# Kernel optimization log

Hardware: AMD Instinct MI355X
Metric: run time of the kernel (lower is better)

Reference implementation:

```python
import jax, jax.numpy as jnp
import numpy as np

TAU = 1.0


def setup_inputs() -> dict:
    key = jax.random.key(0)
    k1, k2 = jax.random.split(key)
    z = jax.random.normal(k1, (131072, 64), dtype=jnp.float32)
    cluster_centers = jax.random.normal(k2, (512, 64), dtype=jnp.float32)
    return {"z": z, "cluster_centers": cluster_centers}


def reference(z, cluster_centers):
    # ||z - c||^2 = ||z||^2 + ||c||^2 - 2 z.c  (avoids the [B,K,D] broadcast tensor)
    z_sq = jnp.sum(z * z, axis=1, keepdims=True)              # [B, 1]
    c_sq = jnp.sum(cluster_centers * cluster_centers, axis=1)  # [K]
    cross = jnp.einsum('bd,kd->bk', z, cluster_centers)        # [B, K]
    dist_sq = z_sq + c_sq[None, :] - 2.0 * cross               # [B, K]
    q = jax.nn.softmax(-dist_sq / TAU, axis=1)                 # [B, K]
    loss = jnp.mean(jnp.sum(q * dist_sq, axis=1))
    return (q, loss)
```

## Files before the change

kernel.cpp:

```cpp
#include <hip/hip_runtime.h>

typedef short bf16x8 __attribute__((ext_vector_type(8)));
typedef float f32x4 __attribute__((ext_vector_type(4)));

#define K_CLUSTERS 512
#define DIM 64
#define ROWS_PER_BLOCK 64

__device__ __forceinline__ unsigned short f32_to_bf16_rne(float f) {
    unsigned int u = __float_as_uint(f);
    u += 0x7fffu + ((u >> 16) & 1u);
    return (unsigned short)(u >> 16);
}
__device__ __forceinline__ float bf16_bits_to_f32(unsigned short h) {
    return __uint_as_float(((unsigned int)h) << 16);
}

__global__ void prep_centers(const float* __restrict__ c,
                             short* __restrict__ c_hi, short* __restrict__ c_lo,
                             float* __restrict__ c_sq, float* __restrict__ loss_out) {
    if (blockIdx.x == 0 && threadIdx.x == 0) loss_out[0] = 0.0f;
    int idx = blockIdx.x * 256 + threadIdx.x;
    float v = c[idx];
    unsigned short h = f32_to_bf16_rne(v);
    float hf = bf16_bits_to_f32(h);
    unsigned short l = f32_to_bf16_rne(v - hf);
    c_hi[idx] = (short)h;
    c_lo[idx] = (short)l;
    float s = v * v;
    #pragma unroll
    for (int off = 1; off < 64; off <<= 1) s += __shfl_xor(s, off, 64);
    if ((threadIdx.x & 63) == 0) c_sq[idx >> 6] = s;
}

#define BARRIER() do {                                      \
    asm volatile("s_waitcnt lgkmcnt(0)" ::: "memory");      \
    __builtin_amdgcn_s_barrier();                           \
} while (0)

__global__ __launch_bounds__(512, 4)
void cluster_kernel(const float* __restrict__ z,
                    const short* __restrict__ c_hi,
                    const short* __restrict__ c_lo,
                    const float* __restrict__ c_sq,
                    float* __restrict__ q_out,
                    float* __restrict__ loss_out,
                    float inv_b) {
    __shared__ __align__(16) short a_hi_s[16][72];
    __shared__ __align__(16) short a_lo_s[16][72];
    __shared__ __align__(16) float2 red_s[8][16];
    __shared__ float wloss_s[8];

    const int tid  = threadIdx.x;
    const int lane = tid & 63;
    const int wave = tid >> 6;
    const int m    = lane & 15;
    const int qd   = lane >> 4;
    const long rb  = (long)blockIdx.x * ROWS_PER_BLOCK;

    bf16x8 bh[4][2], bl[4][2];
    float csq[4];
    #pragma unroll
    for (int t = 0; t < 4; ++t) {
        const int col = wave * 64 + t * 16 + m;
        const long boff = (long)col * DIM + qd * 8;
        #pragma unroll
        for (int kg = 0; kg < 2; ++kg) {
            bh[t][kg] = *(const bf16x8*)(c_hi + boff + kg * 32);
            bl[t][kg] = *(const bf16x8*)(c_lo + boff + kg * 32);
        }
        csq[t] = c_sq[col];
    }

    const float2* zin = (const float2*)(z + rb * DIM);
    const int srow = tid >> 5;
    const int scol = (tid & 31) * 2;

    float lsum = 0.0f;
    float zpart;

    float2 v = zin[tid];
    zpart = v.x * v.x + v.y * v.y;
    {
        unsigned short hx = f32_to_bf16_rne(v.x);
        unsigned short lx = f32_to_bf16_rne(v.x - bf16_bits_to_f32(hx));
        unsigned short hy = f32_to_bf16_rne(v.y);
        unsigned short ly = f32_to_bf16_rne(v.y - bf16_bits_to_f32(hy));
        *(unsigned int*)&a_hi_s[srow][scol] = (unsigned int)hx | ((unsigned int)hy << 16);
        *(unsigned int*)&a_lo_s[srow][scol] = (unsigned int)lx | ((unsigned int)ly << 16);
    }
    BARRIER();

    for (int s = 0; s < ROWS_PER_BLOCK / 16; ++s) {
        float2 vn = v;
        if (s + 1 < ROWS_PER_BLOCK / 16) vn = zin[(s + 1) * 512 + tid];

        bf16x8 ah[2], al[2];
        #pragma unroll
        for (int kg = 0; kg < 2; ++kg) {
            ah[kg] = *(const bf16x8*)&a_hi_s[m][kg * 32 + qd * 8];
            al[kg] = *(const bf16x8*)&a_lo_s[m][kg * 32 + qd * 8];
        }

        f32x4 acc[4];
        #pragma unroll
        for (int t = 0; t < 4; ++t) acc[t] = (f32x4){0.f, 0.f, 0.f, 0.f};
        #pragma unroll
        for (int kg = 0; kg < 2; ++kg) {
            #pragma unroll
            for (int t = 0; t < 4; ++t) {
                acc[t] = __builtin_amdgcn_mfma_f32_16x16x32_bf16(ah[kg], bh[t][kg], acc[t], 0, 0, 0);
                acc[t] = __builtin_amdgcn_mfma_f32_16x16x32_bf16(ah[kg], bl[t][kg], acc[t], 0, 0, 0);
                acc[t] = __builtin_amdgcn_mfma_f32_16x16x32_bf16(al[kg], bh[t][kg], acc[t], 0, 0, 0);
            }
        }

        float dd[4][4];
        #pragma unroll
        for (int t = 0; t < 4; ++t)
            #pragma unroll
            for (int r = 0; r < 4; ++r)
                dd[t][r] = __builtin_fmaf(-2.0f, acc[t][r], csq[t]);

        float mnw[4], sw[4], e[4][4], ped[4];
        #pragma unroll
        for (int r = 0; r < 4; ++r) {
            float mn0 = fminf(fminf(dd[0][r], dd[1][r]), fminf(dd[2][r], dd[3][r]));
            #pragma unroll
            for (int off = 1; off < 16; off <<= 1)
                mn0 = fminf(mn0, __shfl_xor(mn0, off, 64));
            mnw[r] = mn0;
        }
        #pragma unroll
        for (int t = 0; t < 4; ++t)
            #pragma unroll
            for (int r = 0; r < 4; ++r)
                e[t][r] = __expf(mnw[r] - dd[t][r]);
        #pragma unroll
        for (int r = 0; r < 4; ++r) {
            float s0 = (e[0][r] + e[1][r]) + (e[2][r] + e[3][r]);
            #pragma unroll
            for (int off = 1; off < 16; off <<= 1)
                s0 += __shfl_xor(s0, off, 64);
            sw[r] = s0;
            ped[r] = __builtin_fmaf(e[0][r], dd[0][r],
                     __builtin_fmaf(e[1][r], dd[1][r],
                     __builtin_fmaf(e[2][r], dd[2][r], e[3][r] * dd[3][r])));
        }
        if (m == 0) {
            #pragma unroll
            for (int r = 0; r < 4; ++r)
                red_s[wave][qd * 4 + r] = make_float2(mnw[r], sw[r]);
        }
        BARRIER();

        if (s + 1 < ROWS_PER_BLOCK / 16) {
            zpart += vn.x * vn.x + vn.y * vn.y;
            unsigned short hx = f32_to_bf16_rne(vn.x);
            unsigned short lx = f32_to_bf16_rne(vn.x - bf16_bits_to_f32(hx));
            unsigned short hy = f32_to_bf16_rne(vn.y);
            unsigned short ly = f32_to_bf16_rne(vn.y - bf16_bits_to_f32(hy));
            *(unsigned int*)&a_hi_s[srow][scol] = (unsigned int)hx | ((unsigned int)hy << 16);
            *(unsigned int*)&a_lo_s[srow][scol] = (unsigned int)lx | ((unsigned int)ly << 16);
        }

        float mn = red_s[0][m].x;
        #pragma unroll
        for (int w2 = 1; w2 < 8; ++w2) mn = fminf(mn, red_s[w2][m].x);
        float S = 0.0f, msf = 0.0f;
        #pragma unroll
        for (int w2 = 0; w2 < 8; ++w2) {
            float2 p = red_s[w2][m];
            S = __builtin_fmaf(p.y, __expf(mn - p.x), S);
            if (w2 == wave) msf = p.x;
        }
        const float fself = __expf(mn - msf) / S;

        float f4[4];
        #pragma unroll
        for (int r = 0; r < 4; ++r) f4[r] = __shfl(fself, qd * 4 + r, 64);

        const long rbase = rb + (long)s * 16;
        float* orow0 = q_out + (rbase + qd * 4) * K_CLUSTERS + wave * 64 + m;
        #pragma unroll
        for (int r = 0; r < 4; ++r) {
            float* orow = orow0 + (long)r * K_CLUSTERS;
            #pragma unroll
            for (int t = 0; t < 4; ++t) {
                const float qv = e[t][r] * f4[r];
                __builtin_nontemporal_store(qv, orow + t * 16);
            }
            lsum = __builtin_fmaf(f4[r], ped[r], lsum);
        }
        v = vn;
        if (s + 1 < ROWS_PER_BLOCK / 16) BARRIER();
    }

    float tot = lsum + zpart;
    #pragma unroll
    for (int off = 1; off < 64; off <<= 1) tot += __shfl_xor(tot, off, 64);
    if (lane == 0) wloss_s[wave] = tot;
    __syncthreads();
    if (tid == 0) {
        float t0 = 0.f;
        #pragma unroll
        for (int w = 0; w < 8; ++w) t0 += wloss_s[w];
        atomicAdd(loss_out, t0 * inv_b);
    }
}

extern "C" void kernel_launch(void* const* d_in, const int* in_sizes, int n_in,
                              void* d_out, int out_size, void* d_ws, size_t ws_size,
                              hipStream_t stream) {
    const float* z = (const float*)d_in[0];
    const float* c = (const float*)d_in[1];
    const int B = in_sizes[0] / DIM;
    float* q_out = (float*)d_out;
    float* loss_out = q_out + (size_t)B * K_CLUSTERS;

    char* ws = (char*)d_ws;
    short* c_hi = (short*)ws;
    short* c_lo = (short*)(ws + 65536);
    float* c_sq = (float*)(ws + 131072);

    prep_centers<<<(K_CLUSTERS * DIM) / 256, 256, 0, stream>>>(c, c_hi, c_lo, c_sq, loss_out);
    cluster_kernel<<<B / ROWS_PER_BLOCK, 512, 0, stream>>>(z, c_hi, c_lo, c_sq, q_out,
                                                           loss_out, 1.0f / (float)B);
}
```

Baseline: 369.8 us.

## Preload all z subtiles to LDS and double-buffer reductions to drop barrier

All four 16-row z subtiles are converted to bf16 hi/lo and stored in LDS up front, and the per-iteration prefetch/convert is removed. The row-reduction buffer is double-buffered so the trailing barrier in each iteration can go. The final q values are recomputed with a second exp against the block-wide minimum instead of rescaling the stored exponentials, and the loss accumulates q*d directly. The aim is fewer barriers and lower register pressure, at the cost of twice as many exp evaluations and more LDS per block.

Result: faster. 343.0 us (-7.2%).

```diff
diff --git a/kernel.cpp b/kernel.cpp
--- a/kernel.cpp
+++ b/kernel.cpp
@@ -6,6 +6,7 @@
 #define K_CLUSTERS 512
 #define DIM 64
 #define ROWS_PER_BLOCK 64
+#define NSUB 4
 
 __device__ __forceinline__ unsigned short f32_to_bf16_rne(float f) {
     unsigned int u = __float_as_uint(f);
@@ -46,9 +47,9 @@
                     float* __restrict__ q_out,
                     float* __restrict__ loss_out,
                     float inv_b) {
-    __shared__ __align__(16) short a_hi_s[16][72];
-    __shared__ __align__(16) short a_lo_s[16][72];
-    __shared__ __align__(16) float2 red_s[8][16];
+    __shared__ __align__(16) short a_hi_s[NSUB][16][72];
+    __shared__ __align__(16) short a_lo_s[NSUB][16][72];
+    __shared__ __align__(16) float2 red_s[2][8][16];
     __shared__ float wloss_s[8];
 
     const int tid  = threadIdx.x;
@@ -75,31 +76,28 @@
     const float2* zin = (const float2*)(z + rb * DIM);
     const int srow = tid >> 5;
     const int scol = (tid & 31) * 2;
-
-    float lsum = 0.0f;
-    float zpart;
-
-    float2 v = zin[tid];
-    zpart = v.x * v.x + v.y * v.y;
-    {
+    float zpart = 0.0f;
+    #pragma unroll
+    for (int k = 0; k < NSUB; ++k) {
+        float2 v = zin[k * 512 + tid];
+        zpart += v.x * v.x + v.y * v.y;
         unsigned short hx = f32_to_bf16_rne(v.x);
         unsigned short lx = f32_to_bf16_rne(v.x - bf16_bits_to_f32(hx));
         unsigned short hy = f32_to_bf16_rne(v.y);
         unsigned short ly = f32_to_bf16_rne(v.y - bf16_bits_to_f32(hy));
-        *(unsigned int*)&a_hi_s[srow][scol] = (unsigned int)hx | ((unsigned int)hy << 16);
-        *(unsigned int*)&a_lo_s[srow][scol] = (unsigned int)lx | ((unsigned int)ly << 16);
+        *(unsigned int*)&a_hi_s[k][srow][scol] = (unsigned int)hx | ((unsigned int)hy << 16);
+        *(unsigned int*)&a_lo_s[k][srow][scol] = (unsigned int)lx | ((unsigned int)ly << 16);
     }
     BARRIER();
 
-    for (int s = 0; s < ROWS_PER_BLOCK / 16; ++s) {
-        float2 vn = v;
-        if (s + 1 < ROWS_PER_BLOCK / 16) vn = zin[(s + 1) * 512 + tid];
-
+    float lsum = 0.0f;
+
+    for (int s = 0; s < NSUB; ++s) {
         bf16x8 ah[2], al[2];
         #pragma unroll
         for (int kg = 0; kg < 2; ++kg) {
-            ah[kg] = *(const bf16x8*)&a_hi_s[m][kg * 32 + qd * 8];
-            al[kg] = *(const bf16x8*)&a_lo_s[m][kg * 32 + qd * 8];
+            ah[kg] = *(const bf16x8*)&a_hi_s[s][m][kg * 32 + qd * 8];
+            al[kg] = *(const bf16x8*)&a_lo_s[s][m][kg * 32 + qd * 8];
         }
 
         f32x4 acc[4];
@@ -122,7 +120,7 @@
             for (int r = 0; r < 4; ++r)
                 dd[t][r] = __builtin_fmaf(-2.0f, acc[t][r], csq[t]);
 
-        float mnw[4], sw[4], e[4][4], ped[4];
+        float mnw[4], sw4[4];
         #pragma unroll
         for (int r = 0; r < 4; ++r) {
             float mn0 = fminf(fminf(dd[0][r], dd[1][r]), fminf(dd[2][r], dd[3][r]));
@@ -132,68 +130,50 @@
             mnw[r] = mn0;
         }
         #pragma unroll
-        for (int t = 0; t < 4; ++t)
-            #pragma unroll
-            for (int r = 0; r < 4; ++r)
-                e[t][r] = __expf(mnw[r] - dd[t][r]);
-        #pragma unroll
-        for (int r = 0; r < 4; ++r) {
-            float s0 = (e[0][r] + e[1][r]) + (e[2][r] + e[3][r]);
+        for (int r = 0; r < 4; ++r) {
+            float s0 = (__expf(mnw[r] - dd[0][r]) + __expf(mnw[r] - dd[1][r]))
+                     + (__expf(mnw[r] - dd[2][r]) + __expf(mnw[r] - dd[3][r]));
             #pragma unroll
             for (int off = 1; off < 16; off <<= 1)
                 s0 += __shfl_xor(s0, off, 64);
-            sw[r] = s0;
-            ped[r] = __builtin_fmaf(e[0][r], dd[0][r],
-                     __builtin_fmaf(e[1][r], dd[1][r],
-                     __builtin_fmaf(e[2][r], dd[2][r], e[3][r] * dd[3][r])));
+            sw4[r] = s0;
         }
         if (m == 0) {
             #pragma unroll
             for (int r = 0; r < 4; ++r)
-                red_s[wave][qd * 4 + r] = make_float2(mnw[r], sw[r]);
+                red_s[s & 1][wave][qd * 4 + r] = make_float2(mnw[r], sw4[r]);
         }
         BARRIER();
 
-        if (s + 1 < ROWS_PER_BLOCK / 16) {
-            zpart += vn.x * vn.x + vn.y * vn.y;
-            unsigned short hx = f32_to_bf16_rne(vn.x);
-            unsigned short lx = f32_to_bf16_rne(vn.x - bf16_bits_to_f32(hx));
-            unsigned short hy = f32_to_bf16_rne(vn.y);
-            unsigned short ly = f32_to_bf16_rne(vn.y - bf16_bits_to_f32(hy));
-            *(unsigned int*)&a_hi_s[srow][scol] = (unsigned int)hx | ((unsigned int)hy << 16);
-            *(unsigned int*)&a_lo_s[srow][scol] = (unsigned int)lx | ((unsigned int)ly << 16);
-        }
-
-        float mn = red_s[0][m].x;
-        #pragma unroll
-        for (int w2 = 1; w2 < 8; ++w2) mn = fminf(mn, red_s[w2][m].x);
-        float S = 0.0f, msf = 0.0f;
+        float mn = red_s[s & 1][0][m].x;
+        #pragma unroll
+        for (int w2 = 1; w2 < 8; ++w2) mn = fminf(mn, red_s[s & 1][w2][m].x);
+        float S = 0.0f;
         #pragma unroll
         for (int w2 = 0; w2 < 8; ++w2) {
-            float2 p = red_s[w2][m];
+            float2 p = red_s[s & 1][w2][m];
             S = __builtin_fmaf(p.y, __expf(mn - p.x), S);
-            if (w2 == wave) msf = p.x;
-        }
-        const float fself = __expf(mn - msf) / S;
-
-        float f4[4];
-        #pragma unroll
-        for (int r = 0; r < 4; ++r) f4[r] = __shfl(fself, qd * 4 + r, 64);
-
-        const long rbase = rb + (long)s * 16;
-        float* orow0 = q_out + (rbase + qd * 4) * K_CLUSTERS + wave * 64 + m;
+        }
+        const float invS = 1.0f / S;
+
+        float mnr[4], fsr[4];
+        #pragma unroll
+        for (int r = 0; r < 4; ++r) {
+            mnr[r] = __shfl(mn,   qd * 4 + r, 64);
+            fsr[r] = __shfl(invS, qd * 4 + r, 64);
+        }
+
+        float* orow0 = q_out + (rb + (long)s * 16 + qd * 4) * K_CLUSTERS + wave * 64 + m;
         #pragma unroll
         for (int r = 0; r < 4; ++r) {
             float* orow = orow0 + (long)r * K_CLUSTERS;
             #pragma unroll
             for (int t = 0; t < 4; ++t) {
-                const float qv = e[t][r] * f4[r];
+                const float qv = __expf(mnr[r] - dd[t][r]) * fsr[r];
                 __builtin_nontemporal_store(qv, orow + t * 16);
+                lsum = __builtin_fmaf(qv, dd[t][r], lsum);
             }
-            lsum = __builtin_fmaf(f4[r], ped[r], lsum);
-        }
-        v = vn;
-        if (s + 1 < ROWS_PER_BLOCK / 16) BARRIER();
+        }
     }
 
     float tot = lsum + zpart;
```
